# Kernel tuning notes

Measured on AMD Instinct MI355X. Metric: run time of the kernel, lower is better.

The kernel has to match this reference:

```python
import jax, jax.numpy as jnp
import numpy as np

B = 8192          # number of graphs (batch)
N_USERS = 128
N_SERVERS = 8
OUT = N_USERS * N_SERVERS      # output_dim = 1024 edges per graph
IN_DIM = OUT + N_USERS + N_SERVERS  # 1160
HID = 256
NUM_SEG = B * N_USERS          # 1,048,576 segment ids


def seg_softmax(x, idx, num_seg):
    # torch_geometric-style scatter softmax over segments defined by idx.
    m = jax.ops.segment_max(x, idx, num_segments=num_seg)   # [num_seg]
    e = jnp.exp(x - m[idx])
    s = jax.ops.segment_sum(e, idx, num_segments=num_seg)
    return e / s[idx]


def setup_inputs() -> dict:
    key = jax.random.key(0)
    ks = jax.random.split(key, 12)
    u2s_path_loss = jax.random.normal(ks[0], (B, OUT), dtype=jnp.float32)
    user_tasksize = jax.random.uniform(ks[1], (B, N_USERS), dtype=jnp.float32)
    server_comp_resource = jax.random.uniform(ks[2], (B, N_SERVERS), dtype=jnp.float32)
    edge_index = jax.random.randint(ks[3], (2, B * OUT), 0, NUM_SEG, dtype=jnp.int64)
    s = 0.02
    W1 = jax.random.normal(ks[4], (IN_DIM, HID), dtype=jnp.float32) * s
    b1 = jnp.zeros((HID,), dtype=jnp.float32)
    W2 = jax.random.normal(ks[5], (HID, HID), dtype=jnp.float32) * s
    b2 = jnp.zeros((HID,), dtype=jnp.float32)
    W3 = jax.random.normal(ks[6], (HID, HID), dtype=jnp.float32) * s
    b3 = jnp.zeros((HID,), dtype=jnp.float32)
    W4 = jax.random.normal(ks[7], (HID, 3 * OUT), dtype=jnp.float32) * s
    b4 = jnp.zeros((3 * OUT,), dtype=jnp.float32)
    return {"u2s_path_loss": u2s_path_loss, "user_tasksize": user_tasksize,
            "server_comp_resource": server_comp_resource, "edge_index": edge_index,
            "W1": W1, "b1": b1, "W2": W2, "b2": b2, "W3": W3, "b3": b3, "W4": W4, "b4": b4}


def reference(u2s_path_loss, user_tasksize, server_comp_resource, edge_index,
              W1, b1, W2, b2, W3, b3, W4, b4):
    feats = jnp.concatenate([u2s_path_loss, user_tasksize, server_comp_resource], axis=1)
    h = jax.nn.relu(feats @ W1 + b1)
    h = jax.nn.relu(h @ W2 + b2)          # encoder output [B, HID]
    h = jax.nn.relu(h @ W3 + b3)
    sches = h @ W4 + b4                   # [B, 3*OUT]
    idx0 = edge_index[0]
    idx1 = edge_index[1]
    task = seg_softmax(sches[:, :OUT].reshape(-1), idx0, NUM_SEG).reshape(B, OUT)
    power = seg_softmax(sches[:, OUT:2 * OUT].reshape(-1), idx0, NUM_SEG).reshape(B, OUT)
    comp = seg_softmax(sches[:, 2 * OUT:].reshape(-1), idx1, NUM_SEG).reshape(B, OUT)
    return (task, power, comp)
```

## Files before the change

kernel.cpp:

```cpp
#include <hip/hip_runtime.h>
#include <math.h>

#define B_GRAPHS 8192
#define OUT_DIM 1024
#define NU 128
#define NS 8
#define IN_DIM 1160
#define KPAD1 1216
#define HID 256
#define NSEG (B_GRAPHS * NU)
#define EDGES (B_GRAPHS * OUT_DIM)

#define BINS 512
#define SEGS_PER_BIN 2048
#define HALF (EDGES / 2)
#define SCHUNK 8192
#define SBLOCKS (HALF / SCHUNK)
#define EPT (SCHUNK / 256)

typedef __attribute__((ext_vector_type(8))) short short8;
typedef __attribute__((ext_vector_type(4))) float f32x4;

__device__ __forceinline__ unsigned short f2bf(float f) {
    unsigned u = __float_as_uint(f);
    const unsigned r = (u >> 16) & 1u;
    return (unsigned short)((u + 0x7fffu + r) >> 16);
}
__device__ __forceinline__ float bf2f(unsigned short b) {
    return __uint_as_float((unsigned)b << 16);
}

__global__ __launch_bounds__(256) void convert_feats_kernel(
    const float* __restrict__ u2s, const float* __restrict__ usr,
    const float* __restrict__ srv, unsigned short* __restrict__ F)
{
    const int t = blockIdx.x * 256 + threadIdx.x;
    const int row = t / 152;
    const int g = t - row * 152;
    const int col = g * 8;
    float v[8];
    if (g < 128) {
        const float4 a = *(const float4*)&u2s[(size_t)row * OUT_DIM + col];
        const float4 b = *(const float4*)&u2s[(size_t)row * OUT_DIM + col + 4];
        v[0]=a.x; v[1]=a.y; v[2]=a.z; v[3]=a.w; v[4]=b.x; v[5]=b.y; v[6]=b.z; v[7]=b.w;
    } else if (g < 144) {
        const int c = col - OUT_DIM;
        const float4 a = *(const float4*)&usr[(size_t)row * NU + c];
        const float4 b = *(const float4*)&usr[(size_t)row * NU + c + 4];
        v[0]=a.x; v[1]=a.y; v[2]=a.z; v[3]=a.w; v[4]=b.x; v[5]=b.y; v[6]=b.z; v[7]=b.w;
    } else if (g == 144) {
        const float4 a = *(const float4*)&srv[(size_t)row * NS];
        const float4 b = *(const float4*)&srv[(size_t)row * NS + 4];
        v[0]=a.x; v[1]=a.y; v[2]=a.z; v[3]=a.w; v[4]=b.x; v[5]=b.y; v[6]=b.z; v[7]=b.w;
    } else {
        for (int i = 0; i < 8; ++i) v[i] = 0.f;
    }
    unsigned short o[8];
    for (int i = 0; i < 8; ++i) o[i] = f2bf(v[i]);
    *reinterpret_cast<short8*>(&F[(size_t)row * KPAD1 + col]) =
        *reinterpret_cast<const short8*>(o);
}

__global__ __launch_bounds__(256) void convert_wT_kernel(
    const float* __restrict__ W, unsigned short* __restrict__ WT,
    int K, int N, int Kpad)
{
    const int t = blockIdx.x * 256 + threadIdx.x;
    if (t >= N * Kpad) return;
    const int n = t / Kpad;
    const int k = t - n * Kpad;
    WT[t] = (k < K) ? f2bf(W[(size_t)k * N + n]) : (unsigned short)0;
}

template <int EPI>
__global__ __launch_bounds__(256) void gemm_bf16_kernel(
    const unsigned short* __restrict__ A, const unsigned short* __restrict__ BT,
    const float* __restrict__ bias, void* __restrict__ outv, int N, int K)
{
    __shared__ unsigned short As[128 * 64];
    __shared__ unsigned short Bs[64 * 64];

    const int tid = threadIdx.x;
    const int lane = tid & 63;
    const int wid = tid >> 6;
    const int wm = wid >> 1;
    const int wn = wid & 1;
    const int m0 = blockIdx.y * 128;
    const int n0 = blockIdx.x * 64;

    const int srow = lane >> 3;
    const int schunk = lane & 7;
    const int sswz = schunk ^ srow;

    f32x4 acc[4][2];
#pragma unroll
    for (int i = 0; i < 4; ++i)
#pragma unroll
        for (int j = 0; j < 2; ++j) acc[i][j] = (f32x4)0.f;

    for (int k0 = 0; k0 < K; k0 += 64) {
#pragma unroll
        for (int i = 0; i < 4; ++i) {
            const int r = wid * 32 + i * 8 + srow;
            const short8 v = *reinterpret_cast<const short8*>(
                &A[(size_t)(m0 + r) * K + k0 + sswz * 8]);
            *reinterpret_cast<short8*>(&As[r * 64 + schunk * 8]) = v;
        }
#pragma unroll
        for (int i = 0; i < 2; ++i) {
            const int r = wid * 16 + i * 8 + srow;
            const short8 v = *reinterpret_cast<const short8*>(
                &BT[(size_t)(n0 + r) * K + k0 + sswz * 8]);
            *reinterpret_cast<short8*>(&Bs[r * 64 + schunk * 8]) = v;
        }
        __syncthreads();

#pragma unroll
        for (int ks = 0; ks < 2; ++ks) {
            short8 af[4], bf[2];
            const int c = ks * 4 + (lane >> 4);
#pragma unroll
            for (int fm = 0; fm < 4; ++fm) {
                const int r = wm * 64 + fm * 16 + (lane & 15);
                af[fm] = *reinterpret_cast<const short8*>(
                    &As[r * 64 + (c ^ (r & 7)) * 8]);
            }
#pragma unroll
            for (int fn = 0; fn < 2; ++fn) {
                const int r = wn * 32 + fn * 16 + (lane & 15);
                bf[fn] = *reinterpret_cast<const short8*>(
                    &Bs[r * 64 + (c ^ (r & 7)) * 8]);
            }
#pragma unroll
            for (int fm = 0; fm < 4; ++fm)
#pragma unroll
                for (int fn = 0; fn < 2; ++fn)
                    acc[fm][fn] = __builtin_amdgcn_mfma_f32_16x16x32_bf16(
                        af[fm], bf[fn], acc[fm][fn], 0, 0, 0);
        }
        __syncthreads();
    }

#pragma unroll
    for (int fn = 0; fn < 2; ++fn) {
        const int col = n0 + wn * 32 + fn * 16 + (lane & 15);
        const float bv = bias[col];
#pragma unroll
        for (int fm = 0; fm < 4; ++fm) {
            const int rbase = m0 + wm * 64 + fm * 16 + (lane >> 4) * 4;
#pragma unroll
            for (int e = 0; e < 4; ++e) {
                const float v = acc[fm][fn][e] + bv;
                if (EPI == 0) {
                    unsigned short* h = (unsigned short*)outv;
                    h[(size_t)(rbase + e) * N + col] = f2bf(fmaxf(v, 0.f));
                } else {
                    float* out = (float*)outv;
                    const int p = col >> 10;
                    const int w = col & 1023;
                    out[(size_t)p * EDGES + (size_t)(rbase + e) * OUT_DIM + w] =
                        __expf(v);
                }
            }
        }
    }
}

__global__ __launch_bounds__(256) void scatter_sort_kernel(
    const int* __restrict__ idx, const float* __restrict__ vals, int w0,
    unsigned* __restrict__ P, unsigned* __restrict__ offs)
{
    __shared__ unsigned hist[BINS];
    __shared__ unsigned lofs[BINS];
    __shared__ unsigned scanbuf[256];
    __shared__ alignas(16) unsigned recs[SCHUNK];

    const int tid = threadIdx.x;
    const int blk = blockIdx.x;
    const int base = w0 + blk * SCHUNK;

    for (int b = tid; b < BINS; b += 256) hist[b] = 0;
    __syncthreads();

    unsigned rec_r[EPT];
    unsigned short bin_r[EPT];
#pragma unroll
    for (int i = 0; i < EPT; ++i) {
        const int w = base + i * 256 + tid;
        const int seg = idx[w];
        const float e = vals[w];
        bin_r[i] = (unsigned short)(seg >> 11);
        rec_r[i] = ((unsigned)(seg & 2047) << 16) | f2bf(e);
        atomicAdd(&hist[bin_r[i]], 1u);
    }
    __syncthreads();

    const unsigned h0 = hist[2 * tid];
    const unsigned h1 = hist[2 * tid + 1];
    const unsigned pairsum = h0 + h1;
    scanbuf[tid] = pairsum;
    __syncthreads();
    for (int d = 1; d < 256; d <<= 1) {
        const unsigned v = (tid >= d) ? scanbuf[tid - d] : 0u;
        __syncthreads();
        scanbuf[tid] += v;
        __syncthreads();
    }
    const unsigned excl = scanbuf[tid] - pairsum;
    hist[2 * tid] = excl;
    hist[2 * tid + 1] = excl + h0;
    lofs[2 * tid] = 0;
    lofs[2 * tid + 1] = 0;
    offs[(size_t)blk * BINS + 2 * tid] = excl;
    offs[(size_t)blk * BINS + 2 * tid + 1] = excl + h0;
    __syncthreads();

#pragma unroll
    for (int i = 0; i < EPT; ++i) {
        const unsigned p = hist[bin_r[i]] + atomicAdd(&lofs[bin_r[i]], 1u);
        recs[p] = rec_r[i];
    }
    __syncthreads();

    const uint4* rs = reinterpret_cast<const uint4*>(recs);
    uint4* dst = reinterpret_cast<uint4*>(&P[(size_t)blk * SCHUNK]);
#pragma unroll
    for (int i = 0; i < SCHUNK / 1024; ++i)
        dst[i * 256 + tid] = rs[i * 256 + tid];
}

__global__ __launch_bounds__(256) void reduce_sorted_kernel(
    const unsigned* __restrict__ P, const unsigned* __restrict__ offs,
    float* __restrict__ s_self, const float* __restrict__ s_other,
    unsigned* __restrict__ r01, unsigned short* __restrict__ r2, int mode)
{
    __shared__ float sub[SEGS_PER_BIN];
    const int b = blockIdx.x;
    const int tid = threadIdx.x;
    for (int i = tid; i < SEGS_PER_BIN; i += 256) sub[i] = 0.f;
    __syncthreads();

    for (int blk = tid; blk < SBLOCKS; blk += 256) {
        const unsigned st = offs[(size_t)blk * BINS + b];
        const unsigned en =
            (b == BINS - 1) ? SCHUNK : offs[(size_t)blk * BINS + b + 1];
        const unsigned* rec = &P[(size_t)blk * SCHUNK];
        for (unsigned i = st; i < en; ++i) {
            const unsigned r = rec[i];
            atomicAdd(&sub[r >> 16], __uint_as_float(r << 16));
        }
    }
    __syncthreads();

    for (int i = tid; i < SEGS_PER_BIN; i += 256) {
        const int seg = b * SEGS_PER_BIN + i;
        if (mode == 0) {
            s_self[seg] = sub[i];
        } else if (mode == 1) {
            s_self[seg] += sub[i];
        } else if (mode == 2) {
            const float s1f = sub[i] + s_self[seg];
            r01[seg] = ((unsigned)f2bf(1.f / s_other[seg]) << 16) |
                       f2bf(1.f / s1f);
        } else {
            r2[seg] = f2bf(1.f / (sub[i] + s_self[seg]));
        }
    }
}

__global__ __launch_bounds__(256) void segdiv01_kernel(
    float* __restrict__ vals, const int* __restrict__ idx0,
    const unsigned* __restrict__ r01)
{
    const int w4 = (blockIdx.x * 256 + threadIdx.x) * 4;
    if (w4 >= EDGES) return;
    const int4 iv = *reinterpret_cast<const int4*>(&idx0[w4]);
    const int idx[4] = {iv.x, iv.y, iv.z, iv.w};
    float4 a = *reinterpret_cast<const float4*>(&vals[w4]);
    float4 b = *reinterpret_cast<const float4*>(&vals[(size_t)EDGES + w4]);
    float r0[4], r1[4];
#pragma unroll
    for (int j = 0; j < 4; ++j) {
        const unsigned p = r01[idx[j]];
        r0[j] = __uint_as_float(p & 0xffff0000u);
        r1[j] = __uint_as_float(p << 16);
    }
    a.x *= r0[0]; a.y *= r0[1]; a.z *= r0[2]; a.w *= r0[3];
    b.x *= r1[0]; b.y *= r1[1]; b.z *= r1[2]; b.w *= r1[3];
    *reinterpret_cast<float4*>(&vals[w4]) = a;
    *reinterpret_cast<float4*>(&vals[(size_t)EDGES + w4]) = b;
}

__global__ __launch_bounds__(256) void segdiv2_kernel(
    float* __restrict__ vals, const int* __restrict__ idx1,
    const unsigned short* __restrict__ r2)
{
    const int w4 = (blockIdx.x * 256 + threadIdx.x) * 4;
    if (w4 >= EDGES) return;
    const int4 iv = *reinterpret_cast<const int4*>(&idx1[w4]);
    const int idx[4] = {iv.x, iv.y, iv.z, iv.w};
    float4 c = *reinterpret_cast<const float4*>(&vals[2 * (size_t)EDGES + w4]);
    c.x *= bf2f(r2[idx[0]]);
    c.y *= bf2f(r2[idx[1]]);
    c.z *= bf2f(r2[idx[2]]);
    c.w *= bf2f(r2[idx[3]]);
    *reinterpret_cast<float4*>(&vals[2 * (size_t)EDGES + w4]) = c;
}

extern "C" void kernel_launch(void* const* d_in, const int* in_sizes, int n_in,
                              void* d_out, int out_size, void* d_ws,
                              size_t ws_size, hipStream_t stream) {
    const float* u2s = (const float*)d_in[0];
    const float* usr = (const float*)d_in[1];
    const float* srv = (const float*)d_in[2];
    const int* edge = (const int*)d_in[3];
    const float* W1 = (const float*)d_in[4];
    const float* b1 = (const float*)d_in[5];
    const float* W2 = (const float*)d_in[6];
    const float* b2 = (const float*)d_in[7];
    const float* W3 = (const float*)d_in[8];
    const float* b3 = (const float*)d_in[9];
    const float* W4 = (const float*)d_in[10];
    const float* b4 = (const float*)d_in[11];

    const int* idx0 = edge;
    const int* idx1 = edge + EDGES;

    char* ws = (char*)d_ws;
    unsigned short* F = (unsigned short*)ws;
    unsigned short* h1 = (unsigned short*)(ws + 20ull * 1024 * 1024);
    unsigned short* h2 = (unsigned short*)(ws + 24ull * 1024 * 1024);
    unsigned short* h3 = (unsigned short*)(ws + 28ull * 1024 * 1024);
    unsigned short* w1t = (unsigned short*)(ws + 32ull * 1024 * 1024);
    unsigned short* w2t = w1t + (size_t)HID * KPAD1;
    unsigned short* w3t = w2t + (size_t)HID * HID;
    unsigned short* w4t = w3t + (size_t)HID * HID;

    unsigned* P = (unsigned*)ws;
    unsigned* offs = (unsigned*)(ws + 16896ull * 1024);
    float* s0 = (float*)(ws + 20ull * 1024 * 1024);
    float* s1 = (float*)(ws + 24ull * 1024 * 1024);
    float* s2 = (float*)(ws + 28ull * 1024 * 1024);
    unsigned* r01 = (unsigned*)(ws + 32ull * 1024 * 1024);
    unsigned short* r2 = (unsigned short*)(ws + 36ull * 1024 * 1024);

    float* outp = (float*)d_out;
    const dim3 blk(256);

    convert_feats_kernel<<<(B_GRAPHS * 152) / 256, blk, 0, stream>>>(u2s, usr,
                                                                     srv, F);
    convert_wT_kernel<<<(HID * KPAD1 + 255) / 256, blk, 0, stream>>>(
        W1, w1t, IN_DIM, HID, KPAD1);
    convert_wT_kernel<<<(HID * HID + 255) / 256, blk, 0, stream>>>(
        W2, w2t, HID, HID, HID);
    convert_wT_kernel<<<(HID * HID + 255) / 256, blk, 0, stream>>>(
        W3, w3t, HID, HID, HID);
    convert_wT_kernel<<<(3 * OUT_DIM * HID + 255) / 256, blk, 0, stream>>>(
        W4, w4t, HID, 3 * OUT_DIM, HID);

    gemm_bf16_kernel<0><<<dim3(HID / 64, B_GRAPHS / 128), blk, 0, stream>>>(
        F, w1t, b1, h1, HID, KPAD1);
    gemm_bf16_kernel<0><<<dim3(HID / 64, B_GRAPHS / 128), blk, 0, stream>>>(
        h1, w2t, b2, h2, HID, HID);
    gemm_bf16_kernel<0><<<dim3(HID / 64, B_GRAPHS / 128), blk, 0, stream>>>(
        h2, w3t, b3, h3, HID, HID);
    gemm_bf16_kernel<1><<<dim3(3 * OUT_DIM / 64, B_GRAPHS / 128), blk, 0,
                          stream>>>(h3, w4t, b4, outp, 3 * OUT_DIM, HID);

    for (int h = 0; h < 2; ++h) {
        scatter_sort_kernel<<<SBLOCKS, blk, 0, stream>>>(idx0, outp, h * HALF,
                                                         P, offs);
        reduce_sorted_kernel<<<BINS, blk, 0, stream>>>(P, offs, s0, nullptr,
                                                       nullptr, nullptr, h);
    }
    for (int h = 0; h < 2; ++h) {
        scatter_sort_kernel<<<SBLOCKS, blk, 0, stream>>>(
            idx0, outp + (size_t)EDGES, h * HALF, P, offs);
        reduce_sorted_kernel<<<BINS, blk, 0, stream>>>(P, offs, s1, s0, r01,
                                                       nullptr, h == 0 ? 0 : 2);
    }
    for (int h = 0; h < 2; ++h) {
        scatter_sort_kernel<<<SBLOCKS, blk, 0, stream>>>(
            idx1, outp + 2 * (size_t)EDGES, h * HALF, P, offs);
        reduce_sorted_kernel<<<BINS, blk, 0, stream>>>(P, offs, s2, nullptr,
                                                       nullptr, r2,
                                                       h == 0 ? 0 : 3);
    }

    segdiv01_kernel<<<EDGES / 1024, blk, 0, stream>>>(outp, idx0, r01);
    segdiv2_kernel<<<EDGES / 1024, blk, 0, stream>>>(outp, idx1, r2);
}
```

Before: 476.0 us.

## Fuse task and power segment-sum sort passes sharing idx0 into one pass

The task and power softmaxes share the same segment index, so their two scatter-sort and reduce passes are merged into one. Each sorted record becomes 64 bits, holding both bf16 exp values plus the local segment id, and the reducer accumulates two shared-memory sums at once. This removes a full pass of index reads, histogramming and sort launches, at the cost of a doubled shared-memory record buffer (lower occupancy) and wider record traffic. Loads and stores of streamed data also switch to nontemporal hints, and the workspace layout is rearranged to fit the larger buffers.

Result: no change. 475.4 us (-0.1%).

```diff
diff --git a/kernel.cpp b/kernel.cpp
--- a/kernel.cpp
+++ b/kernel.cpp
@@ -20,6 +20,7 @@
 
 typedef __attribute__((ext_vector_type(8))) short short8;
 typedef __attribute__((ext_vector_type(4))) float f32x4;
+typedef __attribute__((ext_vector_type(4))) int i32x4;
 
 __device__ __forceinline__ unsigned short f2bf(float f) {
     unsigned u = __float_as_uint(f);
@@ -166,14 +167,15 @@
     }
 }
 
-__global__ __launch_bounds__(256) void scatter_sort_kernel(
-    const int* __restrict__ idx, const float* __restrict__ vals, int w0,
-    unsigned* __restrict__ P, unsigned* __restrict__ offs)
+__global__ __launch_bounds__(256) void scatter01_sort_kernel(
+    const int* __restrict__ idx, const float* __restrict__ v0,
+    const float* __restrict__ v1, int w0,
+    unsigned long long* __restrict__ P, unsigned* __restrict__ offs)
 {
     __shared__ unsigned hist[BINS];
     __shared__ unsigned lofs[BINS];
     __shared__ unsigned scanbuf[256];
-    __shared__ alignas(16) unsigned recs[SCHUNK];
+    __shared__ alignas(16) unsigned long long recs[SCHUNK];
 
     const int tid = threadIdx.x;
     const int blk = blockIdx.x;
@@ -182,16 +184,18 @@
     for (int b = tid; b < BINS; b += 256) hist[b] = 0;
     __syncthreads();
 
-    unsigned rec_r[EPT];
-    unsigned short bin_r[EPT];
+    unsigned val_r[EPT];
+    unsigned meta_r[EPT];
 #pragma unroll
     for (int i = 0; i < EPT; ++i) {
         const int w = base + i * 256 + tid;
-        const int seg = idx[w];
-        const float e = vals[w];
-        bin_r[i] = (unsigned short)(seg >> 11);
-        rec_r[i] = ((unsigned)(seg & 2047) << 16) | f2bf(e);
-        atomicAdd(&hist[bin_r[i]], 1u);
+        const int seg = __builtin_nontemporal_load(&idx[w]);
+        const float e0 = __builtin_nontemporal_load(&v0[w]);
+        const float e1 = __builtin_nontemporal_load(&v1[w]);
+        const unsigned bin = (unsigned)seg >> 11;
+        meta_r[i] = (bin << 16) | ((unsigned)seg & 2047u);
+        val_r[i] = ((unsigned)f2bf(e0) << 16) | f2bf(e1);
+        atomicAdd(&hist[bin], 1u);
     }
     __syncthreads();
 
@@ -217,6 +221,109 @@
 
 #pragma unroll
     for (int i = 0; i < EPT; ++i) {
+        const unsigned bin = meta_r[i] >> 16;
+        const unsigned p = hist[bin] + atomicAdd(&lofs[bin], 1u);
+        recs[p] = ((unsigned long long)(meta_r[i] & 2047u) << 32) | val_r[i];
+    }
+    __syncthreads();
+
+    const ulonglong2* rs = reinterpret_cast<const ulonglong2*>(recs);
+    ulonglong2* dst = reinterpret_cast<ulonglong2*>(&P[(size_t)blk * SCHUNK]);
+#pragma unroll
+    for (int i = 0; i < SCHUNK / 512; ++i)
+        dst[i * 256 + tid] = rs[i * 256 + tid];
+}
+
+__global__ __launch_bounds__(256) void reduce01_sorted_kernel(
+    const unsigned long long* __restrict__ P, const unsigned* __restrict__ offs,
+    float2* __restrict__ s01, unsigned* __restrict__ r01, int last)
+{
+    __shared__ float sub0[SEGS_PER_BIN];
+    __shared__ float sub1[SEGS_PER_BIN];
+    const int b = blockIdx.x;
+    const int tid = threadIdx.x;
+    for (int i = tid; i < SEGS_PER_BIN; i += 256) { sub0[i] = 0.f; sub1[i] = 0.f; }
+    __syncthreads();
+
+    for (int blk = tid; blk < SBLOCKS; blk += 256) {
+        const unsigned st = offs[(size_t)blk * BINS + b];
+        const unsigned en =
+            (b == BINS - 1) ? SCHUNK : offs[(size_t)blk * BINS + b + 1];
+        const unsigned long long* rec = &P[(size_t)blk * SCHUNK];
+        for (unsigned i = st; i < en; ++i) {
+            const unsigned long long r = rec[i];
+            const int sl = (int)(r >> 32);
+            const unsigned lo = (unsigned)r;
+            atomicAdd(&sub0[sl], __uint_as_float(lo & 0xffff0000u));
+            atomicAdd(&sub1[sl], __uint_as_float(lo << 16));
+        }
+    }
+    __syncthreads();
+
+    for (int i = tid; i < SEGS_PER_BIN; i += 256) {
+        const int seg = b * SEGS_PER_BIN + i;
+        if (!last) {
+            s01[seg] = make_float2(sub0[i], sub1[i]);
+        } else {
+            const float2 p = s01[seg];
+            const float s0f = sub0[i] + p.x;
+            const float s1f = sub1[i] + p.y;
+            r01[seg] = ((unsigned)f2bf(1.f / s0f) << 16) | f2bf(1.f / s1f);
+        }
+    }
+}
+
+__global__ __launch_bounds__(256) void scatter2_sort_kernel(
+    const int* __restrict__ idx, const float* __restrict__ vals, int w0,
+    unsigned* __restrict__ P, unsigned* __restrict__ offs)
+{
+    __shared__ unsigned hist[BINS];
+    __shared__ unsigned lofs[BINS];
+    __shared__ unsigned scanbuf[256];
+    __shared__ alignas(16) unsigned recs[SCHUNK];
+
+    const int tid = threadIdx.x;
+    const int blk = blockIdx.x;
+    const int base = w0 + blk * SCHUNK;
+
+    for (int b = tid; b < BINS; b += 256) hist[b] = 0;
+    __syncthreads();
+
+    unsigned rec_r[EPT];
+    unsigned short bin_r[EPT];
+#pragma unroll
+    for (int i = 0; i < EPT; ++i) {
+        const int w = base + i * 256 + tid;
+        const int seg = __builtin_nontemporal_load(&idx[w]);
+        const float e = __builtin_nontemporal_load(&vals[w]);
+        bin_r[i] = (unsigned short)((unsigned)seg >> 11);
+        rec_r[i] = (((unsigned)seg & 2047u) << 16) | f2bf(e);
+        atomicAdd(&hist[bin_r[i]], 1u);
+    }
+    __syncthreads();
+
+    const unsigned h0 = hist[2 * tid];
+    const unsigned h1 = hist[2 * tid + 1];
+    const unsigned pairsum = h0 + h1;
+    scanbuf[tid] = pairsum;
+    __syncthreads();
+    for (int d = 1; d < 256; d <<= 1) {
+        const unsigned v = (tid >= d) ? scanbuf[tid - d] : 0u;
+        __syncthreads();
+        scanbuf[tid] += v;
+        __syncthreads();
+    }
+    const unsigned excl = scanbuf[tid] - pairsum;
+    hist[2 * tid] = excl;
+    hist[2 * tid + 1] = excl + h0;
+    lofs[2 * tid] = 0;
+    lofs[2 * tid + 1] = 0;
+    offs[(size_t)blk * BINS + 2 * tid] = excl;
+    offs[(size_t)blk * BINS + 2 * tid + 1] = excl + h0;
+    __syncthreads();
+
+#pragma unroll
+    for (int i = 0; i < EPT; ++i) {
         const unsigned p = hist[bin_r[i]] + atomicAdd(&lofs[bin_r[i]], 1u);
         recs[p] = rec_r[i];
     }
@@ -229,10 +336,9 @@
         dst[i * 256 + tid] = rs[i * 256 + tid];
 }
 
-__global__ __launch_bounds__(256) void reduce_sorted_kernel(
+__global__ __launch_bounds__(256) void reduce2_sorted_kernel(
     const unsigned* __restrict__ P, const unsigned* __restrict__ offs,
-    float* __restrict__ s_self, const float* __restrict__ s_other,
-    unsigned* __restrict__ r01, unsigned short* __restrict__ r2, int mode)
+    float* __restrict__ s2, unsigned short* __restrict__ r2, int last)
 {
     __shared__ float sub[SEGS_PER_BIN];
     const int b = blockIdx.x;
@@ -254,17 +360,8 @@
 
     for (int i = tid; i < SEGS_PER_BIN; i += 256) {
         const int seg = b * SEGS_PER_BIN + i;
-        if (mode == 0) {
-            s_self[seg] = sub[i];
-        } else if (mode == 1) {
-            s_self[seg] += sub[i];
-        } else if (mode == 2) {
-            const float s1f = sub[i] + s_self[seg];
-            r01[seg] = ((unsigned)f2bf(1.f / s_other[seg]) << 16) |
-                       f2bf(1.f / s1f);
-        } else {
-            r2[seg] = f2bf(1.f / (sub[i] + s_self[seg]));
-        }
+        if (!last) s2[seg] = sub[i];
+        else       r2[seg] = f2bf(1.f / (sub[i] + s2[seg]));
     }
 }
 
@@ -274,21 +371,21 @@
 {
     const int w4 = (blockIdx.x * 256 + threadIdx.x) * 4;
     if (w4 >= EDGES) return;
-    const int4 iv = *reinterpret_cast<const int4*>(&idx0[w4]);
-    const int idx[4] = {iv.x, iv.y, iv.z, iv.w};
-    float4 a = *reinterpret_cast<const float4*>(&vals[w4]);
-    float4 b = *reinterpret_cast<const float4*>(&vals[(size_t)EDGES + w4]);
-    float r0[4], r1[4];
+    const i32x4 iv =
+        __builtin_nontemporal_load(reinterpret_cast<const i32x4*>(&idx0[w4]));
+    f32x4 a =
+        __builtin_nontemporal_load(reinterpret_cast<const f32x4*>(&vals[w4]));
+    f32x4 b = __builtin_nontemporal_load(
+        reinterpret_cast<const f32x4*>(&vals[(size_t)EDGES + w4]));
 #pragma unroll
     for (int j = 0; j < 4; ++j) {
-        const unsigned p = r01[idx[j]];
-        r0[j] = __uint_as_float(p & 0xffff0000u);
-        r1[j] = __uint_as_float(p << 16);
-    }
-    a.x *= r0[0]; a.y *= r0[1]; a.z *= r0[2]; a.w *= r0[3];
-    b.x *= r1[0]; b.y *= r1[1]; b.z *= r1[2]; b.w *= r1[3];
-    *reinterpret_cast<float4*>(&vals[w4]) = a;
-    *reinterpret_cast<float4*>(&vals[(size_t)EDGES + w4]) = b;
+        const unsigned p = r01[iv[j]];
+        a[j] *= __uint_as_float(p & 0xffff0000u);
+        b[j] *= __uint_as_float(p << 16);
+    }
+    __builtin_nontemporal_store(a, reinterpret_cast<f32x4*>(&vals[w4]));
+    __builtin_nontemporal_store(
+        b, reinterpret_cast<f32x4*>(&vals[(size_t)EDGES + w4]));
 }
 
 __global__ __launch_bounds__(256) void segdiv2_kernel(
@@ -297,14 +394,14 @@
 {
     const int w4 = (blockIdx.x * 256 + threadIdx.x) * 4;
     if (w4 >= EDGES) return;
-    const int4 iv = *reinterpret_cast<const int4*>(&idx1[w4]);
-    const int idx[4] = {iv.x, iv.y, iv.z, iv.w};
-    float4 c = *reinterpret_cast<const float4*>(&vals[2 * (size_t)EDGES + w4]);
-    c.x *= bf2f(r2[idx[0]]);
-    c.y *= bf2f(r2[idx[1]]);
-    c.z *= bf2f(r2[idx[2]]);
-    c.w *= bf2f(r2[idx[3]]);
-    *reinterpret_cast<float4*>(&vals[2 * (size_t)EDGES + w4]) = c;
+    const i32x4 iv =
+        __builtin_nontemporal_load(reinterpret_cast<const i32x4*>(&idx1[w4]));
+    f32x4 c = __builtin_nontemporal_load(
+        reinterpret_cast<const f32x4*>(&vals[2 * (size_t)EDGES + w4]));
+#pragma unroll
+    for (int j = 0; j < 4; ++j) c[j] *= bf2f(r2[iv[j]]);
+    __builtin_nontemporal_store(
+        c, reinterpret_cast<f32x4*>(&vals[2 * (size_t)EDGES + w4]));
 }
 
 extern "C" void kernel_launch(void* const* d_in, const int* in_sizes, int n_in,
@@ -331,18 +428,18 @@
     unsigned short* h1 = (unsigned short*)(ws + 20ull * 1024 * 1024);
     unsigned short* h2 = (unsigned short*)(ws + 24ull * 1024 * 1024);
     unsigned short* h3 = (unsigned short*)(ws + 28ull * 1024 * 1024);
-    unsigned short* w1t = (unsigned short*)(ws + 32ull * 1024 * 1024);
+    unsigned short* w1t = (unsigned short*)(ws + 41ull * 1024 * 1024);
     unsigned short* w2t = w1t + (size_t)HID * KPAD1;
     unsigned short* w3t = w2t + (size_t)HID * HID;
     unsigned short* w4t = w3t + (size_t)HID * HID;
 
-    unsigned* P = (unsigned*)ws;
-    unsigned* offs = (unsigned*)(ws + 16896ull * 1024);
-    float* s0 = (float*)(ws + 20ull * 1024 * 1024);
-    float* s1 = (float*)(ws + 24ull * 1024 * 1024);
-    float* s2 = (float*)(ws + 28ull * 1024 * 1024);
-    unsigned* r01 = (unsigned*)(ws + 32ull * 1024 * 1024);
-    unsigned short* r2 = (unsigned short*)(ws + 36ull * 1024 * 1024);
+    unsigned long long* P64 = (unsigned long long*)ws;
+    unsigned* P32 = (unsigned*)ws;
+    unsigned* offs = (unsigned*)(ws + 32ull * 1024 * 1024);
+    float2* s01 = (float2*)(ws + 33ull * 1024 * 1024);
+    float* s2 = (float*)(ws + 33ull * 1024 * 1024);
+    unsigned* r01 = (unsigned*)(ws + 41ull * 1024 * 1024);
+    unsigned short* r2 = (unsigned short*)(ws + 45ull * 1024 * 1024);
 
     float* outp = (float*)d_out;
     const dim3 blk(256);
@@ -368,23 +465,15 @@
                           stream>>>(h3, w4t, b4, outp, 3 * OUT_DIM, HID);
 
     for (int h = 0; h < 2; ++h) {
-        scatter_sort_kernel<<<SBLOCKS, blk, 0, stream>>>(idx0, outp, h * HALF,
-                                                         P, offs);
-        reduce_sorted_kernel<<<BINS, blk, 0, stream>>>(P, offs, s0, nullptr,
-                                                       nullptr, nullptr, h);
+        scatter01_sort_kernel<<<SBLOCKS, blk, 0, stream>>>(
+            idx0, outp, outp + (size_t)EDGES, h * HALF, P64, offs);
+        reduce01_sorted_kernel<<<BINS, blk, 0, stream>>>(P64, offs, s01, r01,
+                                                         h);
     }
     for (int h = 0; h < 2; ++h) {
-        scatter_sort_kernel<<<SBLOCKS, blk, 0, stream>>>(
-            idx0, outp + (size_t)EDGES, h * HALF, P, offs);
-        reduce_sorted_kernel<<<BINS, blk, 0, stream>>>(P, offs, s1, s0, r01,
-                                                       nullptr, h == 0 ? 0 : 2);
-    }
-    for (int h = 0; h < 2; ++h) {
-        scatter_sort_kernel<<<SBLOCKS, blk, 0, stream>>>(
-            idx1, outp + 2 * (size_t)EDGES, h * HALF, P, offs);
-        reduce_sorted_kernel<<<BINS, blk, 0, stream>>>(P, offs, s2, nullptr,
-                                                       nullptr, r2,
-                                                       h == 0 ? 0 : 3);
+        scatter2_sort_kernel<<<SBLOCKS, blk, 0, stream>>>(
+            idx1, outp + 2 * (size_t)EDGES, h * HALF, P32, offs);
+        reduce2_sorted_kernel<<<BINS, blk, 0, stream>>>(P32, offs, s2, r2, h);
     }
 
     segdiv01_kernel<<<EDGES / 1024, blk, 0, stream>>>(outp, idx0, r01);
```
